# Kernel optimization log

Measured on AMD Instinct MI355X. Metric: run time of the kernel, lower is better.

The kernel has to match this reference:

```python
import jax, jax.numpy as jnp
import numpy as np
import math

VOCAB, E, CTX, DK, DH, H, HID, L = 50257, 768, 2048, 64, 64, 12, 3072, 2
B, S = 2, 2048
NEG_INF = -1e30


def _pos_encoding(seq_len, dim):
    pos = jnp.arange(seq_len, dtype=jnp.float32)[:, None]
    i = jnp.arange(dim, dtype=jnp.float32)[None, :]
    angle = pos / jnp.power(10000.0, 2.0 * i / dim)
    return jnp.where(jnp.arange(dim)[None, :] % 2 == 0, jnp.sin(angle), jnp.cos(angle))


def _layernorm(x, scale, bias, eps=1e-5):
    mu = jnp.mean(x, axis=-1, keepdims=True)
    var = jnp.var(x, axis=-1, keepdims=True)
    return (x - mu) * jax.lax.rsqrt(var + eps) * scale + bias


def setup_inputs() -> dict:
    key = jax.random.key(0)
    ks = jax.random.split(key, 10)
    s = 0.02  # init scale for stability
    return {
        "tokens": jax.random.randint(ks[0], (B, S), 0, VOCAB),
        "emb": jax.random.normal(ks[1], (VOCAB, E), jnp.float32) * s,
        "ln1_s": jnp.ones((L, E), jnp.float32),
        "ln1_b": jnp.zeros((L, E), jnp.float32),
        "Wq": jax.random.normal(ks[2], (L, H, E, DK), jnp.float32) * s,
        "bq": jnp.zeros((L, H, DK), jnp.float32),
        "Wk": jax.random.normal(ks[3], (L, H, E, DK), jnp.float32) * s,
        "bk": jnp.zeros((L, H, DK), jnp.float32),
        "Wv": jax.random.normal(ks[4], (L, H, E, DH), jnp.float32) * s,
        "bv": jnp.zeros((L, H, DH), jnp.float32),
        "ln2_s": jnp.ones((L, E), jnp.float32),
        "ln2_b": jnp.zeros((L, E), jnp.float32),
        "W1": jax.random.normal(ks[5], (L, E, HID), jnp.float32) * s,
        "b1": jnp.zeros((L, HID), jnp.float32),
        "W2": jax.random.normal(ks[6], (L, HID, E), jnp.float32) * s,
        "b2": jnp.zeros((L, E), jnp.float32),
        "Wout": jax.random.normal(ks[7], (E, VOCAB), jnp.float32) * s,
        "bout": jnp.zeros((VOCAB,), jnp.float32),
    }


def reference(tokens, emb, ln1_s, ln1_b, Wq, bq, Wk, bk, Wv, bv, ln2_s, ln2_b, W1, b1, W2, b2, Wout, bout):
    seq = tokens.shape[1]
    x = emb[tokens] + _pos_encoding(seq, E)  # [B,S,E]
    causal = jnp.triu(jnp.full((seq, seq), NEG_INF, jnp.float32), k=1)
    for l in range(Wq.shape[0]):
        # pre-norm on attention input; note residual adds to the NORMALIZED h (faithful to original)
        h = _layernorm(x, ln1_s[l], ln1_b[l])
        q = jnp.einsum('bse,hed->bhsd', h, Wq[l]) + bq[l][None, :, None, :]
        k = jnp.einsum('bse,hed->bhsd', h, Wk[l]) + bk[l][None, :, None, :]
        v = jnp.einsum('bse,hed->bhsd', h, Wv[l]) + bv[l][None, :, None, :]
        scores = jnp.einsum('bhsd,bhtd->bhst', q, k) / math.sqrt(DK) + causal
        w = jax.nn.softmax(scores, axis=-1)  # [B,H,S,S]
        o = jnp.einsum('bhst,bhtd->bhsd', w, v)  # [B,H,S,DH]
        o = jnp.transpose(o, (0, 2, 1, 3)).reshape(o.shape[0], seq, H * DH)  # concat heads
        x = h + o
        h2 = _layernorm(x, ln2_s[l], ln2_b[l])
        x = h2 + jnp.einsum('bsf,fe->bse', jax.nn.relu(jnp.einsum('bse,ef->bsf', h2, W1[l]) + b1[l]), W2[l]) + b2[l]
    logits = jnp.einsum('bse,ev->bsv', x, Wout) + bout  # training-mode output
    return logits
```

## Files before the change

kernel.cpp:

```cpp
#include <hip/hip_runtime.h>
#include <stdint.h>

#define DEV static __device__ __forceinline__

typedef unsigned short u16;
typedef __attribute__((ext_vector_type(8))) short short8;
typedef __attribute__((ext_vector_type(4))) float f32x4;

#define B_     2
#define S_     2048
#define E_     768
#define H_     12
#define L_     2
#define HID_   3072
#define VOCAB_ 50257
#define VPAD_  50432
#define M_     4096
#define NQKV_  2304

DEV u16 f2bf(float f) {
  union { float f; unsigned u; } x; x.f = f;
  unsigned r = x.u + 0x7fffu + ((x.u >> 16) & 1u);
  return (u16)(r >> 16);
}

DEV void gload16(const void* g, void* lds) {
  __builtin_amdgcn_global_load_lds(
      (const __attribute__((address_space(1))) unsigned int*)g,
      (__attribute__((address_space(3))) unsigned int*)lds, 16, 0, 0);
}

__global__ __launch_bounds__(256) void k_transp(
    const float* __restrict__ in, u16* __restrict__ out,
    int R, int Cin, long long ib1, long long ib2, long long ob1, long long ob2, int zdiv)
{
  __shared__ float t[32][33];
  const int z = blockIdx.z;
  const float* ib = in  + (size_t)(z / zdiv) * ib1 + (size_t)(z % zdiv) * ib2;
  u16*         ob = out + (size_t)(z / zdiv) * ob1 + (size_t)(z % zdiv) * ob2;
  const int c0 = blockIdx.x * 32, r0 = blockIdx.y * 32;
  const int tx = threadIdx.x, ty = threadIdx.y;
#pragma unroll
  for (int i = 0; i < 4; i++) {
    const int c = c0 + tx, r = r0 + ty + i * 8;
    t[ty + i * 8][tx] = (c < Cin) ? ib[(size_t)r * Cin + c] : 0.f;
  }
  __syncthreads();
#pragma unroll
  for (int i = 0; i < 4; i++) {
    const int orow = c0 + ty + i * 8;
    ob[(size_t)orow * R + r0 + tx] = f2bf(t[tx][ty + i * 8]);
  }
}

__global__ __launch_bounds__(256) void k_pack_bias(
    const float* __restrict__ bq, const float* __restrict__ bk,
    const float* __restrict__ bv, float* __restrict__ bqkv)
{
  const int i = blockIdx.x * 256 + threadIdx.x;
  if (i >= L_ * NQKV_) return;
  const int l = i / NQKV_, n = i % NQKV_;
  const float* s = (n < 768) ? bq : (n < 1536) ? bk : bv;
  bqkv[i] = s[l * 768 + (n % 768)];
}

__global__ __launch_bounds__(256) void k_embed(
    const int* __restrict__ tok, const float* __restrict__ emb, float* __restrict__ x)
{
  const int idx = blockIdx.x * 256 + threadIdx.x;
  const int e = idx % E_;
  const int row = idx / E_;
  const int s = row & (S_ - 1);
  const int t = tok[row];
  const float ang = (float)s * expf((float)e * (-2.0f / 768.f) * 9.210340371976184f);
  const float pe = (e & 1) ? cosf(ang) : sinf(ang);
  x[idx] = emb[(size_t)t * E_ + e] + pe;
}

__global__ __launch_bounds__(256) void k_ln(
    const float* __restrict__ xin, const float* __restrict__ sc,
    const float* __restrict__ bi, float* __restrict__ hout, u16* __restrict__ hb)
{
  const int row  = blockIdx.x * 4 + (threadIdx.x >> 6);
  const int lane = threadIdx.x & 63;
  const float* xr = xin + (size_t)row * E_;
  float v[12];
  float s = 0.f;
#pragma unroll
  for (int i = 0; i < 12; i++) { v[i] = xr[i * 64 + lane]; s += v[i]; }
#pragma unroll
  for (int o = 1; o < 64; o <<= 1) s += __shfl_xor(s, o);
  const float mu = s * (1.f / 768.f);
  float s2 = 0.f;
#pragma unroll
  for (int i = 0; i < 12; i++) { const float d = v[i] - mu; s2 += d * d; }
#pragma unroll
  for (int o = 1; o < 64; o <<= 1) s2 += __shfl_xor(s2, o);
  const float rs = rsqrtf(s2 * (1.f / 768.f) + 1e-5f);
#pragma unroll
  for (int i = 0; i < 12; i++) {
    const int c = i * 64 + lane;
    const float ov = (v[i] - mu) * rs * sc[c] + bi[c];
    hout[(size_t)row * E_ + c] = ov;
    hb[(size_t)row * E_ + c]   = f2bf(ov);
  }
}

template <int EPI>
__global__ __launch_bounds__(256) void k_gemm(
    const u16* __restrict__ A, const u16* __restrict__ Bt,
    const float* __restrict__ bias, const float* __restrict__ res,
    void* __restrict__ outp, u16* __restrict__ out2, int Mm, int Nn, int Kk)
{
  __shared__ __align__(16) u16 As[128 * 32];
  __shared__ __align__(16) u16 Bs[128 * 32];
  const int tid  = threadIdx.x;
  const int lane = tid & 63;
  const int wid  = tid >> 6;
  const int wr = wid >> 1, wc = wid & 1;
  const int m0 = blockIdx.y * 128, n0 = blockIdx.x * 128;

  const u16* Ab = A  + (size_t)m0 * Kk;
  const u16* Bb = Bt + (size_t)n0 * Kk;

  f32x4 acc[4][4];
#pragma unroll
  for (int i = 0; i < 4; i++)
#pragma unroll
    for (int j = 0; j < 4; j++) acc[i][j] = (f32x4){0.f, 0.f, 0.f, 0.f};

  const int c0 = tid, c1 = 256 + tid;
  const int a0row = c0 >> 2, a0k = (c0 & 3) * 8;
  const int a1row = c1 >> 2, a1k = (c1 & 3) * 8;
  const int nk = Kk >> 5;
  const int kg = (lane >> 4) * 8;
  const int arow = wr * 64 + (lane & 15);
  const int brow = wc * 64 + (lane & 15);

  for (int kt = 0; kt < nk; ++kt) {
    const int kof = kt * 32;
    __syncthreads();
    gload16(Ab + (size_t)a0row * Kk + kof + a0k, &As[c0 * 8]);
    gload16(Ab + (size_t)a1row * Kk + kof + a1k, &As[c1 * 8]);
    gload16(Bb + (size_t)a0row * Kk + kof + a0k, &Bs[c0 * 8]);
    gload16(Bb + (size_t)a1row * Kk + kof + a1k, &Bs[c1 * 8]);
    asm volatile("s_waitcnt vmcnt(0)" ::: "memory");
    __syncthreads();
    short8 af[4], bf[4];
#pragma unroll
    for (int i = 0; i < 4; i++) af[i] = *(const short8*)&As[(arow + i * 16) * 32 + kg];
#pragma unroll
    for (int i = 0; i < 4; i++) bf[i] = *(const short8*)&Bs[(brow + i * 16) * 32 + kg];
#pragma unroll
    for (int mi = 0; mi < 4; mi++)
#pragma unroll
      for (int ni = 0; ni < 4; ni++)
        acc[mi][ni] = __builtin_amdgcn_mfma_f32_16x16x32_bf16(af[mi], bf[ni], acc[mi][ni], 0, 0, 0);
  }

  const int colg = lane & 15;
  const int rowg = (lane >> 4) * 4;
#pragma unroll
  for (int mi = 0; mi < 4; mi++) {
#pragma unroll
    for (int ni = 0; ni < 4; ni++) {
      const int col = n0 + wc * 64 + ni * 16 + colg;
      const float bb = bias[col];
#pragma unroll
      for (int r = 0; r < 4; r++) {
        const int row = m0 + wr * 64 + mi * 16 + rowg + r;
        float v = acc[mi][ni][r] + bb;
        if (EPI == 0)      ((u16*)outp)[(size_t)row * Nn + col] = f2bf(v);
        else if (EPI == 1) ((u16*)outp)[(size_t)row * Nn + col] = f2bf(fmaxf(v, 0.f));
        else if (EPI == 2) ((float*)outp)[(size_t)row * Nn + col] = v + res[(size_t)row * Nn + col];
        else if (EPI == 4) {
          const float o = v + res[(size_t)row * Nn + col];
          ((float*)outp)[(size_t)row * Nn + col] = o;
          out2[(size_t)row * Nn + col] = f2bf(o);
        }
      }
    }
  }
}

__global__ __launch_bounds__(512, 2) void k_gemm256(
    const u16* __restrict__ A, const u16* __restrict__ Bt,
    const float* __restrict__ bias, float* __restrict__ out,
    int Nn, int Kk, int nreal, int mpx)
{
  __shared__ __align__(16) u16 As[2][256 * 64];
  __shared__ __align__(16) u16 Bs[2][256 * 64];

  const int id = blockIdx.x;
  const int xcd = id & 7;
  const int j = id >> 3;
  const int m0 = (xcd * mpx + (j % mpx)) * 256;
  const int n0 = (j / mpx) * 256;

  const int tid = threadIdx.x, lane = tid & 63, w = tid >> 6;
  const int wr = w >> 2, wcn = w & 3;
  const int l15 = lane & 15, ks = lane >> 4;

  const u16* Ab = A  + (size_t)m0 * Kk;
  const u16* Bb = Bt + (size_t)n0 * Kk;

  const int srow  = lane >> 3;
  const int sslot = ((lane & 7) ^ srow) * 8;
  const int wrow  = w * 8;

  f32x4 acc[8][4];
#pragma unroll
  for (int i = 0; i < 8; i++)
#pragma unroll
    for (int n = 0; n < 4; n++) acc[i][n] = (f32x4){0.f, 0.f, 0.f, 0.f};

  const int nk = Kk >> 6;

  auto stA = [&](int b, int R, int ko) {
    gload16(Ab + (size_t)(R + wrow + srow) * Kk + ko + sslot,      &As[b][(R + wrow) * 64]);
    gload16(Ab + (size_t)(R + 64 + wrow + srow) * Kk + ko + sslot, &As[b][(R + 64 + wrow) * 64]);
  };
  auto stB = [&](int b, int R, int ko) {
    gload16(Bb + (size_t)(R + wrow + srow) * Kk + ko + sslot,      &Bs[b][(R + wrow) * 64]);
    gload16(Bb + (size_t)(R + 64 + wrow + srow) * Kk + ko + sslot, &Bs[b][(R + 64 + wrow) * 64]);
  };

  short8 af[4], bf[4];
  auto ldA = [&](int b, int fmh, int ksub) {
#pragma unroll
    for (int i = 0; i < 4; i++) {
      const int r = wr * 128 + fmh * 64 + i * 16 + l15;
      const int sl = ((ksub * 4 + ks) ^ (r & 7)) * 8;
      af[i] = *(const short8*)&As[b][r * 64 + sl];
    }
  };
  auto ldB = [&](int b, int ksub) {
#pragma unroll
    for (int n = 0; n < 4; n++) {
      const int r = wcn * 64 + n * 16 + l15;
      const int sl = ((ksub * 4 + ks) ^ (r & 7)) * 8;
      bf[n] = *(const short8*)&Bs[b][r * 64 + sl];
    }
  };
  auto mm = [&](int fmh) {
    __builtin_amdgcn_s_setprio(1);
#pragma unroll
    for (int i = 0; i < 4; i++)
#pragma unroll
      for (int n = 0; n < 4; n++)
        acc[fmh * 4 + i][n] =
            __builtin_amdgcn_mfma_f32_16x16x32_bf16(af[i], bf[n], acc[fmh * 4 + i][n], 0, 0, 0);
    __builtin_amdgcn_s_setprio(0);
  };

#define BAR_() do { __builtin_amdgcn_sched_barrier(0); __builtin_amdgcn_s_barrier(); \
                    __builtin_amdgcn_sched_barrier(0); } while (0)
#define LGKM_() do { asm volatile("s_waitcnt lgkmcnt(0)" ::: "memory"); \
                     __builtin_amdgcn_sched_barrier(0); } while (0)

  stA(0, 0, 0); stA(0, 128, 0); stB(0, 0, 0); stB(0, 128, 0);
  if (nk > 1) {
    stA(1, 0, 64); stA(1, 128, 64);
    asm volatile("s_waitcnt vmcnt(4)" ::: "memory");
  } else {
    asm volatile("s_waitcnt vmcnt(0)" ::: "memory");
  }
  BAR_();

  for (int t = 0; t < nk; ++t) {
    const int cur = t & 1;
    const int kon = (t + 1) << 6;
    ldA(cur, 0, 0); ldB(cur, 0);
    if (t + 1 < nk) stB(cur ^ 1, 0, kon);
    BAR_(); LGKM_(); mm(0); BAR_();
    ldA(cur, 1, 0);
    if (t + 1 < nk) stB(cur ^ 1, 128, kon);
    BAR_(); LGKM_(); mm(1); BAR_();
    ldA(cur, 0, 1); ldB(cur, 1);
    BAR_(); LGKM_(); mm(0); BAR_();
    ldA(cur, 1, 1);
    BAR_(); LGKM_(); mm(1); BAR_();
    if (t + 2 < nk) {
      const int kon2 = (t + 2) << 6;
      stA(cur, 0, kon2); stA(cur, 128, kon2);
      asm volatile("s_waitcnt vmcnt(4)" ::: "memory");
    } else {
      asm volatile("s_waitcnt vmcnt(0)" ::: "memory");
    }
    BAR_();
  }
#undef BAR_
#undef LGKM_

#pragma unroll
  for (int fm = 0; fm < 8; fm++) {
    const int row = m0 + wr * 128 + fm * 16 + ks * 4;
#pragma unroll
    for (int n = 0; n < 4; n++) {
      const int col = n0 + wcn * 64 + n * 16 + l15;
      if (col < nreal) {
        const float bb = bias[col];
#pragma unroll
        for (int r = 0; r < 4; r++)
          out[(size_t)(row + r) * nreal + col] = acc[fm][n][r] + bb;
      }
    }
  }
}

__global__ __launch_bounds__(256) void k_attn(
    const u16* __restrict__ qkv, const float* __restrict__ h, float* __restrict__ x)
{
  const int tid = threadIdx.x, lane = tid & 63, wid = tid >> 6;
  const int bh = blockIdx.y, b = bh / H_, hh = bh % H_;
  const int q0 = blockIdx.x * 64;
  const int qw = q0 + wid * 16;

  __shared__ __align__(16) u16 Ks[32 * 72];
  __shared__ __align__(16) u16 Vt[64 * 40];
  __shared__ __align__(16) u16 Ps[4][16 * 40];

  const size_t rowbase = (size_t)b * S_;
  const u16* qb = qkv + rowbase * NQKV_ + hh * 64;
  const u16* kb = qb + 768;
  const u16* vb = qb + 1536;

  const int l15 = lane & 15;
  const int kg  = (lane >> 4) * 8;

  short8 qf0, qf1;
  {
    const u16* g = qb + (size_t)(qw + l15) * NQKV_ + kg;
    qf0 = *(const short8*)g;
    qf1 = *(const short8*)(g + 32);
  }

  f32x4 ov[4];
#pragma unroll
  for (int i = 0; i < 4; i++) ov[i] = (f32x4){0.f, 0.f, 0.f, 0.f};
  float mr[4], lr[4];
#pragma unroll
  for (int r = 0; r < 4; r++) { mr[r] = -1e30f; lr[r] = 0.f; }

  const int srow = tid >> 3, sc8 = (tid & 7) * 8;
  const int nkt = q0 / 32 + 2;
  for (int kt = 0; kt < nkt; ++kt) {
    __syncthreads();
    {
      const size_t gr = (size_t)(kt * 32 + srow) * NQKV_;
      const uint4 kd = *(const uint4*)(kb + gr + sc8);
      *(uint4*)&Ks[srow * 72 + sc8] = kd;
      const uint4 vd = *(const uint4*)(vb + gr + sc8);
      const u16* ve = (const u16*)&vd;
#pragma unroll
      for (int j = 0; j < 8; j++) Vt[(sc8 + j) * 40 + srow] = ve[j];
    }
    __syncthreads();
    if (kt * 32 <= qw + 15) {
      f32x4 s0 = (f32x4){0.f, 0.f, 0.f, 0.f}, s1 = (f32x4){0.f, 0.f, 0.f, 0.f};
      const short8 k00 = *(const short8*)&Ks[l15 * 72 + kg];
      const short8 k01 = *(const short8*)&Ks[l15 * 72 + 32 + kg];
      const short8 k10 = *(const short8*)&Ks[(16 + l15) * 72 + kg];
      const short8 k11 = *(const short8*)&Ks[(16 + l15) * 72 + 32 + kg];
      s0 = __builtin_amdgcn_mfma_f32_16x16x32_bf16(qf0, k00, s0, 0, 0, 0);
      s0 = __builtin_amdgcn_mfma_f32_16x16x32_bf16(qf1, k01, s0, 0, 0, 0);
      s1 = __builtin_amdgcn_mfma_f32_16x16x32_bf16(qf0, k10, s1, 0, 0, 0);
      s1 = __builtin_amdgcn_mfma_f32_16x16x32_bf16(qf1, k11, s1, 0, 0, 0);

      const int qrow0 = qw + (lane >> 4) * 4;
      const int kc0 = kt * 32 + l15, kc1 = kc0 + 16;
      float p0[4], p1[4], mt[4];
#pragma unroll
      for (int r = 0; r < 4; r++) {
        const int qr = qrow0 + r;
        p0[r] = (kc0 <= qr) ? s0[r] * 0.125f : -1e30f;
        p1[r] = (kc1 <= qr) ? s1[r] * 0.125f : -1e30f;
        mt[r] = fmaxf(p0[r], p1[r]);
      }
#pragma unroll
      for (int r = 0; r < 4; r++) {
#pragma unroll
        for (int off = 1; off < 16; off <<= 1) mt[r] = fmaxf(mt[r], __shfl_xor(mt[r], off));
      }
      float al[4];
#pragma unroll
      for (int r = 0; r < 4; r++) {
        const float mn = fmaxf(mr[r], mt[r]);
        al[r] = __expf(mr[r] - mn);
        mr[r] = mn;
        p0[r] = __expf(p0[r] - mn);
        p1[r] = __expf(p1[r] - mn);
      }
      float ps[4];
#pragma unroll
      for (int r = 0; r < 4; r++) ps[r] = p0[r] + p1[r];
#pragma unroll
      for (int r = 0; r < 4; r++) {
#pragma unroll
        for (int off = 1; off < 16; off <<= 1) ps[r] += __shfl_xor(ps[r], off);
        lr[r] = lr[r] * al[r] + ps[r];
      }
#pragma unroll
      for (int dt = 0; dt < 4; dt++)
#pragma unroll
        for (int r = 0; r < 4; r++) ov[dt][r] *= al[r];

      u16* pw = &Ps[wid][0];
#pragma unroll
      for (int r = 0; r < 4; r++) {
        const int pr = (lane >> 4) * 4 + r;
        pw[pr * 40 + l15]      = f2bf(p0[r]);
        pw[pr * 40 + 16 + l15] = f2bf(p1[r]);
      }
      const short8 pa = *(const short8*)&pw[l15 * 40 + kg];
#pragma unroll
      for (int dt = 0; dt < 4; dt++) {
        const short8 vf = *(const short8*)&Vt[(dt * 16 + l15) * 40 + kg];
        ov[dt] = __builtin_amdgcn_mfma_f32_16x16x32_bf16(pa, vf, ov[dt], 0, 0, 0);
      }
    }
  }
#pragma unroll
  for (int dt = 0; dt < 4; dt++) {
#pragma unroll
    for (int r = 0; r < 4; r++) {
      const int qr = qw + (lane >> 4) * 4 + r;
      const int col = hh * 64 + dt * 16 + l15;
      const size_t idx = (rowbase + qr) * (size_t)E_ + col;
      x[idx] = h[idx] + ov[dt][r] / lr[r];
    }
  }
}

extern "C" void kernel_launch(void* const* d_in, const int* in_sizes, int n_in,
                              void* d_out, int out_size, void* d_ws, size_t ws_size,
                              hipStream_t stream)
{
  const int*   tok  = (const int*)  d_in[0];
  const float* emb  = (const float*)d_in[1];
  const float* ln1s = (const float*)d_in[2];
  const float* ln1b = (const float*)d_in[3];
  const float* Wq   = (const float*)d_in[4];
  const float* bq   = (const float*)d_in[5];
  const float* Wk   = (const float*)d_in[6];
  const float* bk   = (const float*)d_in[7];
  const float* Wv   = (const float*)d_in[8];
  const float* bv   = (const float*)d_in[9];
  const float* ln2s = (const float*)d_in[10];
  const float* ln2b = (const float*)d_in[11];
  const float* W1   = (const float*)d_in[12];
  const float* b1   = (const float*)d_in[13];
  const float* W2   = (const float*)d_in[14];
  const float* b2   = (const float*)d_in[15];
  const float* Wo   = (const float*)d_in[16];
  const float* bo   = (const float*)d_in[17];
  float* out = (float*)d_out;

  char* p = (char*)d_ws;
  float* xf    = (float*)p; p += (size_t)M_ * E_ * 4;
  float* hf    = (float*)p; p += (size_t)M_ * E_ * 4;
  u16*   hb    = (u16*)p;   p += (size_t)M_ * E_ * 2;
  u16*   xb    = (u16*)p;   p += (size_t)M_ * E_ * 2;
  u16*   midb  = (u16*)p;   p += (size_t)M_ * HID_ * 2;
  u16*   qkvb  = (u16*)p;   p += (size_t)M_ * NQKV_ * 2;
  u16*   Wqkvt = (u16*)p;   p += (size_t)L_ * NQKV_ * E_ * 2;
  u16*   W1t   = (u16*)p;   p += (size_t)L_ * HID_ * E_ * 2;
  u16*   W2t   = (u16*)p;   p += (size_t)L_ * E_ * HID_ * 2;
  u16*   Wot   = (u16*)p;   p += (size_t)VPAD_ * E_ * 2;
  float* bqkv  = (float*)p; p += (size_t)L_ * NQKV_ * 4;

  const dim3 tb32(32, 8, 1);
  k_transp<<<dim3(HID_ / 32, E_ / 32, L_), tb32, 0, stream>>>(
      W1, W1t, E_, HID_, (long long)E_ * HID_, 0, (long long)HID_ * E_, 0, 1);
  k_transp<<<dim3(E_ / 32, HID_ / 32, L_), tb32, 0, stream>>>(
      W2, W2t, HID_, E_, (long long)HID_ * E_, 0, (long long)E_ * HID_, 0, 1);
  k_transp<<<dim3(VPAD_ / 32, E_ / 32, 1), tb32, 0, stream>>>(
      Wo, Wot, E_, VOCAB_, 0, 0, 0, 0, 1);
  k_transp<<<dim3(2, E_ / 32, L_ * H_), tb32, 0, stream>>>(
      Wq, Wqkvt, E_, 64, (long long)H_ * E_ * 64, (long long)E_ * 64,
      (long long)NQKV_ * E_, 64LL * E_, H_);
  k_transp<<<dim3(2, E_ / 32, L_ * H_), tb32, 0, stream>>>(
      Wk, Wqkvt + 768 * E_, E_, 64, (long long)H_ * E_ * 64, (long long)E_ * 64,
      (long long)NQKV_ * E_, 64LL * E_, H_);
  k_transp<<<dim3(2, E_ / 32, L_ * H_), tb32, 0, stream>>>(
      Wv, Wqkvt + 1536 * E_, E_, 64, (long long)H_ * E_ * 64, (long long)E_ * 64,
      (long long)NQKV_ * E_, 64LL * E_, H_);
  k_pack_bias<<<18, 256, 0, stream>>>(bq, bk, bv, bqkv);
  k_embed<<<(M_ * E_) / 256, 256, 0, stream>>>(tok, emb, xf);

  for (int l = 0; l < L_; ++l) {
    k_ln<<<M_ / 4, 256, 0, stream>>>(xf, ln1s + l * E_, ln1b + l * E_, hf, hb);
    k_gemm<0><<<dim3(NQKV_ / 128, M_ / 128), 256, 0, stream>>>(
        hb, Wqkvt + (size_t)l * NQKV_ * E_, bqkv + l * NQKV_, nullptr, qkvb, nullptr,
        M_, NQKV_, E_);
    k_attn<<<dim3(S_ / 64, B_ * H_), 256, 0, stream>>>(qkvb, hf, xf);
    k_ln<<<M_ / 4, 256, 0, stream>>>(xf, ln2s + l * E_, ln2b + l * E_, hf, hb);
    k_gemm<1><<<dim3(HID_ / 128, M_ / 128), 256, 0, stream>>>(
        hb, W1t + (size_t)l * HID_ * E_, b1 + l * HID_, nullptr, midb, nullptr,
        M_, HID_, E_);
    if (l == L_ - 1) {
      k_gemm<4><<<dim3(E_ / 128, M_ / 128), 256, 0, stream>>>(
          midb, W2t + (size_t)l * E_ * HID_, b2 + l * E_, hf, xf, xb, M_, E_, HID_);
    } else {
      k_gemm<2><<<dim3(E_ / 128, M_ / 128), 256, 0, stream>>>(
          midb, W2t + (size_t)l * E_ * HID_, b2 + l * E_, hf, xf, nullptr, M_, E_, HID_);
    }
  }
  k_gemm256<<<dim3(8 * 2 * (VPAD_ / 256)), 512, 0, stream>>>(
      xb, Wot, bo, out, VPAD_, E_, VOCAB_, 2);
}
```

Baseline: 1.322 ms.

## Enlarge attention key tile to 128 and swizzle transposed V in LDS

The flash-attention kernel now processes 128 keys per iteration instead of 32, running online softmax over 8 score column tiles per step. This cuts the number of block barriers, max/sum shuffle reductions and rescale passes per key, and applies the causal mask only on the final tile. The transposed V tile uses an XOR swizzle to reduce LDS bank conflicts. In exchange, LDS use and register pressure rise, and up to 128 keys of work past the diagonal are computed and masked instead of 32.

```diff
diff --git a/kernel.cpp b/kernel.cpp
--- a/kernel.cpp
+++ b/kernel.cpp
@@ -316,9 +316,9 @@
   const int q0 = blockIdx.x * 64;
   const int qw = q0 + wid * 16;
 
-  __shared__ __align__(16) u16 Ks[32 * 72];
-  __shared__ __align__(16) u16 Vt[64 * 40];
-  __shared__ __align__(16) u16 Ps[4][16 * 40];
+  __shared__ __align__(16) u16 Ks[128 * 72];
+  __shared__ __align__(16) u16 Vt[64 * 136];
+  __shared__ __align__(16) u16 Ps[4][16 * 136];
 
   const size_t rowbase = (size_t)b * S_;
   const u16* qb = qkv + rowbase * NQKV_ + hh * 64;
@@ -326,7 +326,9 @@
   const u16* vb = qb + 1536;
 
   const int l15 = lane & 15;
-  const int kg  = (lane >> 4) * 8;
+  const int ks  = lane >> 4;
+  const int kg  = ks * 8;
+  const int ks4 = ks * 4;
 
   short8 qf0, qf1;
   {
@@ -342,89 +344,103 @@
 #pragma unroll
   for (int r = 0; r < 4; r++) { mr[r] = -1e30f; lr[r] = 0.f; }
 
-  const int srow = tid >> 3, sc8 = (tid & 7) * 8;
-  const int nkt = q0 / 32 + 2;
+  const int srow = tid >> 3;
+  const int sc8  = (tid & 7) * 8;
+  const int g8   = tid & 7;
+  const int nkt  = (q0 >> 7) + 1;
+
   for (int kt = 0; kt < nkt; ++kt) {
+    const int kbase = kt << 7;
     __syncthreads();
-    {
-      const size_t gr = (size_t)(kt * 32 + srow) * NQKV_;
+#pragma unroll
+    for (int pass = 0; pass < 4; ++pass) {
+      const int r = srow + pass * 32;
+      const size_t gr = (size_t)(kbase + r) * NQKV_;
       const uint4 kd = *(const uint4*)(kb + gr + sc8);
-      *(uint4*)&Ks[srow * 72 + sc8] = kd;
+      *(uint4*)&Ks[r * 72 + sc8] = kd;
       const uint4 vd = *(const uint4*)(vb + gr + sc8);
       const u16* ve = (const u16*)&vd;
-#pragma unroll
-      for (int j = 0; j < 8; j++) Vt[(sc8 + j) * 40 + srow] = ve[j];
+      const int sb = (((r >> 3) ^ g8) << 3) + (r & 7);
+#pragma unroll
+      for (int jj = 0; jj < 8; jj++) Vt[(sc8 + jj) * 136 + sb] = ve[jj];
     }
     __syncthreads();
-    if (kt * 32 <= qw + 15) {
-      f32x4 s0 = (f32x4){0.f, 0.f, 0.f, 0.f}, s1 = (f32x4){0.f, 0.f, 0.f, 0.f};
-      const short8 k00 = *(const short8*)&Ks[l15 * 72 + kg];
-      const short8 k01 = *(const short8*)&Ks[l15 * 72 + 32 + kg];
-      const short8 k10 = *(const short8*)&Ks[(16 + l15) * 72 + kg];
-      const short8 k11 = *(const short8*)&Ks[(16 + l15) * 72 + 32 + kg];
-      s0 = __builtin_amdgcn_mfma_f32_16x16x32_bf16(qf0, k00, s0, 0, 0, 0);
-      s0 = __builtin_amdgcn_mfma_f32_16x16x32_bf16(qf1, k01, s0, 0, 0, 0);
-      s1 = __builtin_amdgcn_mfma_f32_16x16x32_bf16(qf0, k10, s1, 0, 0, 0);
-      s1 = __builtin_amdgcn_mfma_f32_16x16x32_bf16(qf1, k11, s1, 0, 0, 0);
-
-      const int qrow0 = qw + (lane >> 4) * 4;
-      const int kc0 = kt * 32 + l15, kc1 = kc0 + 16;
-      float p0[4], p1[4], mt[4];
+
+    const bool last = (kt == nkt - 1);
+    float p[8][4], mt[4];
+#pragma unroll
+    for (int r = 0; r < 4; r++) mt[r] = -1e30f;
+#pragma unroll
+    for (int ct = 0; ct < 8; ++ct) {
+      f32x4 s = (f32x4){0.f, 0.f, 0.f, 0.f};
+      const short8 kf0 = *(const short8*)&Ks[(ct * 16 + l15) * 72 + kg];
+      const short8 kf1 = *(const short8*)&Ks[(ct * 16 + l15) * 72 + 32 + kg];
+      s = __builtin_amdgcn_mfma_f32_16x16x32_bf16(qf0, kf0, s, 0, 0, 0);
+      s = __builtin_amdgcn_mfma_f32_16x16x32_bf16(qf1, kf1, s, 0, 0, 0);
+      const int kc = kbase + ct * 16 + l15;
 #pragma unroll
       for (int r = 0; r < 4; r++) {
-        const int qr = qrow0 + r;
-        p0[r] = (kc0 <= qr) ? s0[r] * 0.125f : -1e30f;
-        p1[r] = (kc1 <= qr) ? s1[r] * 0.125f : -1e30f;
-        mt[r] = fmaxf(p0[r], p1[r]);
+        float v = s[r] * 0.125f;
+        if (last && kc > qw + ks4 + r) v = -1e30f;
+        p[ct][r] = v;
+        mt[r] = fmaxf(mt[r], v);
       }
+    }
+#pragma unroll
+    for (int r = 0; r < 4; r++) {
+#pragma unroll
+      for (int off = 1; off < 16; off <<= 1) mt[r] = fmaxf(mt[r], __shfl_xor(mt[r], off));
+    }
+    float al[4], ps[4];
+#pragma unroll
+    for (int r = 0; r < 4; r++) {
+      const float mn = fmaxf(mr[r], mt[r]);
+      al[r] = __expf(mr[r] - mn);
+      mr[r] = mn;
+      ps[r] = 0.f;
+    }
+#pragma unroll
+    for (int ct = 0; ct < 8; ++ct)
 #pragma unroll
       for (int r = 0; r < 4; r++) {
-#pragma unroll
-        for (int off = 1; off < 16; off <<= 1) mt[r] = fmaxf(mt[r], __shfl_xor(mt[r], off));
+        p[ct][r] = __expf(p[ct][r] - mr[r]);
+        ps[r] += p[ct][r];
       }
-      float al[4];
-#pragma unroll
-      for (int r = 0; r < 4; r++) {
-        const float mn = fmaxf(mr[r], mt[r]);
-        al[r] = __expf(mr[r] - mn);
-        mr[r] = mn;
-        p0[r] = __expf(p0[r] - mn);
-        p1[r] = __expf(p1[r] - mn);
-      }
-      float ps[4];
-#pragma unroll
-      for (int r = 0; r < 4; r++) ps[r] = p0[r] + p1[r];
-#pragma unroll
-      for (int r = 0; r < 4; r++) {
-#pragma unroll
-        for (int off = 1; off < 16; off <<= 1) ps[r] += __shfl_xor(ps[r], off);
-        lr[r] = lr[r] * al[r] + ps[r];
-      }
-#pragma unroll
-      for (int dt = 0; dt < 4; dt++)
-#pragma unroll
-        for (int r = 0; r < 4; r++) ov[dt][r] *= al[r];
-
-      u16* pw = &Ps[wid][0];
-#pragma unroll
-      for (int r = 0; r < 4; r++) {
-        const int pr = (lane >> 4) * 4 + r;
-        pw[pr * 40 + l15]      = f2bf(p0[r]);
-        pw[pr * 40 + 16 + l15] = f2bf(p1[r]);
-      }
-      const short8 pa = *(const short8*)&pw[l15 * 40 + kg];
+#pragma unroll
+    for (int r = 0; r < 4; r++) {
+#pragma unroll
+      for (int off = 1; off < 16; off <<= 1) ps[r] += __shfl_xor(ps[r], off);
+      lr[r] = lr[r] * al[r] + ps[r];
+    }
+#pragma unroll
+    for (int dt = 0; dt < 4; dt++)
+#pragma unroll
+      for (int r = 0; r < 4; r++) ov[dt][r] *= al[r];
+
+    u16* pw = &Ps[wid][0];
+#pragma unroll
+    for (int ct = 0; ct < 8; ++ct)
+#pragma unroll
+      for (int r = 0; r < 4; r++)
+        pw[(ks4 + r) * 136 + ct * 16 + l15] = f2bf(p[ct][r]);
+#pragma unroll
+    for (int c = 0; c < 4; ++c) {
+      const short8 pa = *(const short8*)&pw[l15 * 136 + c * 32 + kg];
 #pragma unroll
       for (int dt = 0; dt < 4; dt++) {
-        const short8 vf = *(const short8*)&Vt[(dt * 16 + l15) * 40 + kg];
+        const int d = dt * 16 + l15;
+        const int sb = (((c * 4 + ks) ^ ((d >> 3) & 7)) << 3);
+        const short8 vf = *(const short8*)&Vt[d * 136 + sb];
         ov[dt] = __builtin_amdgcn_mfma_f32_16x16x32_bf16(pa, vf, ov[dt], 0, 0, 0);
       }
     }
   }
+
 #pragma unroll
   for (int dt = 0; dt < 4; dt++) {
 #pragma unroll
     for (int r = 0; r < 4; r++) {
-      const int qr = qw + (lane >> 4) * 4 + r;
+      const int qr = qw + ks4 + r;
       const int col = hh * 64 + dt * 16 + l15;
       const size_t idx = (rowbase + qr) * (size_t)E_ + col;
       x[idx] = h[idx] + ov[dt][r] / lr[r];
```

Result: faster. 1.187 ms (-10.2%).
